# Kernel tuning notes

Hardware: AMD Instinct MI355X
Metric: run time of the kernel (lower is better)

The kernel has to match this reference:

```python
import jax, jax.numpy as jnp
import numpy as np

DIM = 512
EPS = 1e-08
LN_EPS = 1e-05  # torch LayerNorm default


def layer_norm(x, g, b):
    mu = jnp.mean(x, axis=-1, keepdims=True)
    var = jnp.mean(jnp.square(x - mu), axis=-1, keepdims=True)
    return (x - mu) * jax.lax.rsqrt(var + LN_EPS) * g + b


def setup_inputs() -> dict:
    key = jax.random.key(0)
    ks = jax.random.split(key, 10)
    B, NQ, NK, D = 8, 1024, 2048, DIM
    s = 1.0 / np.sqrt(D)
    return {
        "inputs": jax.random.normal(ks[0], (B, NQ, D), jnp.float32),
        "context": jax.random.normal(ks[1], (B, NK, D), jnp.float32),
        "ln_in_g": jnp.ones((D,), jnp.float32),
        "ln_in_b": jnp.zeros((D,), jnp.float32),
        "ln_ctx_g": jnp.ones((D,), jnp.float32),
        "ln_ctx_b": jnp.zeros((D,), jnp.float32),
        "Wq": jax.random.uniform(ks[2], (D, D), jnp.float32, -s, s),
        "bq": jax.random.uniform(ks[3], (D,), jnp.float32, -s, s),
        "Wk": jax.random.uniform(ks[4], (D, D), jnp.float32, -s, s),
        "bk": jax.random.uniform(ks[5], (D,), jnp.float32, -s, s),
        "Wv": jax.random.uniform(ks[6], (D, D), jnp.float32, -s, s),
        "bv": jax.random.uniform(ks[7], (D,), jnp.float32, -s, s),
    }


def reference(inputs, context, ln_in_g, ln_in_b, ln_ctx_g, ln_ctx_b, Wq, bq, Wk, bk, Wv, bv):
    x = layer_norm(inputs, ln_in_g, ln_in_b)
    c = layer_norm(context, ln_ctx_g, ln_ctx_b)
    q = x @ Wq.T + bq  # [B, Nq, D]
    k = c @ Wk.T + bk  # [B, Nk, D]
    v = c @ Wv.T + bv  # [B, Nk, D]
    scale = DIM ** (-0.5)
    dots = jnp.einsum('bid,bjd->bij', q, k) * scale  # [B, Nq, Nk]
    attn = jax.nn.softmax(dots, axis=1) + EPS  # softmax over query axis
    attn = attn / jnp.sum(attn, axis=2, keepdims=True)  # renorm over key axis
    updates = jnp.einsum('bjd,bij->bid', v, attn)
    return updates
```

## Files before the change

kernel.cpp:

```cpp
#include <hip/hip_runtime.h>

using u16 = unsigned short;
typedef __attribute__((ext_vector_type(8))) short short8;
typedef __attribute__((ext_vector_type(4))) float floatx4;

#define NQ 1024
#define NK 2048
#define DD 512

__device__ __forceinline__ u16 f2bf(float f) {
  union { float f; unsigned u; } x; x.f = f;
  unsigned r = (x.u + 0x7fffu + ((x.u >> 16) & 1u)) >> 16;
  return (u16)r;
}
__device__ __forceinline__ float bf2f(u16 u) {
  union { unsigned u; float f; } x; x.u = ((unsigned)u) << 16; return x.f;
}
__device__ __forceinline__ float wave_sum(float v) {
#pragma unroll
  for (int off = 32; off > 0; off >>= 1) v += __shfl_down(v, off, 64);
  return v;
}
__device__ __forceinline__ void gload16(const u16* g, const u16* l) {
  __builtin_amdgcn_global_load_lds(
      (const __attribute__((address_space(1))) void*)g,
      (__attribute__((address_space(3))) void*)l, 16, 0, 0);
}

__global__ __launch_bounds__(256) void ln_prep(
    const float* __restrict__ X1, const float* __restrict__ G1,
    const float* __restrict__ B1, u16* __restrict__ Y1,
    const float* __restrict__ X2, const float* __restrict__ G2,
    const float* __restrict__ B2, u16* __restrict__ Y2,
    const float* __restrict__ Wq, const float* __restrict__ Wk,
    const float* __restrict__ Wv, u16* __restrict__ wqb,
    u16* __restrict__ wkb, u16* __restrict__ wvb, float* __restrict__ Zero) {
  int row = blockIdx.x;
  const int t = threadIdx.x;
  if (row >= 24576) {
    int bx = row - 24576;
    if (bx < 768) {
      const float* src = bx < 256 ? Wq : (bx < 512 ? Wk : Wv);
      u16* dst = bx < 256 ? wqb : (bx < 512 ? wkb : wvb);
      int i = ((bx & 255) * 256 + t) * 4;
      float4 v = *(const float4*)(src + i);
      ushort4 o;
      o.x = f2bf(v.x); o.y = f2bf(v.y); o.z = f2bf(v.z); o.w = f2bf(v.w);
      *(ushort4*)(dst + i) = o;
    } else {
      int i = ((bx - 768) * 256 + t) * 4;
      float4 z = {0.f, 0.f, 0.f, 0.f};
      *(float4*)(Zero + i) = z;
    }
    return;
  }
  const float *X, *G, *Bv; u16* Y;
  if (row < 8192) { X = X1; G = G1; Bv = B1; Y = Y1; }
  else { row -= 8192; X = X2; G = G2; Bv = B2; Y = Y2; }
  const float2 v = ((const float2*)(X + (long)row * DD))[t];
  float s = v.x + v.y, ss = v.x * v.x + v.y * v.y;
  __shared__ float red[8];
  float a = wave_sum(s), b = wave_sum(ss);
  if ((t & 63) == 0) { red[t >> 6] = a; red[4 + (t >> 6)] = b; }
  __syncthreads();
  float tot = red[0] + red[1] + red[2] + red[3];
  float tss = red[4] + red[5] + red[6] + red[7];
  float mu = tot * (1.f / DD);
  float var = tss * (1.f / DD) - mu * mu;
  float rs = rsqrtf(var + 1e-5f);
  float2 g2 = ((const float2*)G)[t];
  float2 b2 = ((const float2*)Bv)[t];
  ushort2 o;
  o.x = f2bf((v.x - mu) * rs * g2.x + b2.x);
  o.y = f2bf((v.y - mu) * rs * g2.y + b2.y);
  ((ushort2*)(Y + (long)row * DD))[t] = o;
}

__global__ __launch_bounds__(256) void gemm_bt(
    const u16* A, const u16* B, const float* bias, void* Cout,
    const u16* A2, const u16* B2, const float* bias2, void* Cout2,
    int K, long sAb, long sBb, long sCb, int ldC,
    float scale, int epi, float* aux0, const float* aux1) {
  __shared__ u16 lA[128 * 64];
  __shared__ u16 lB[128 * 64];
  __shared__ float colred[128];

  int m0, n0, bz;
  if (epi == 3) {
    bz = blockIdx.x; m0 = blockIdx.z * 128; n0 = blockIdx.y * 128;
  } else {
    bz = blockIdx.z; m0 = blockIdx.x * 128; n0 = blockIdx.y * 128;
    if (A2 != nullptr && blockIdx.x >= 64) {
      A = A2; B = B2; bias = bias2; Cout = Cout2;
      m0 = (blockIdx.x - 64) * 128;
    }
  }
  A += (long)bz * sAb;
  B += (long)bz * sBb;
  const int t = threadIdx.x, wave = t >> 6, lane = t & 63;
  const int fm = lane & 15, fq = lane >> 4;
  const int wm = (wave >> 1) * 64, wn = (wave & 1) * 64;

  const int srow = t >> 3;
  const int swz = ((t & 7) ^ (srow & 7)) * 8;
  const u16* gA = A + (long)(m0 + srow) * K + swz;
  const u16* gB = B + (long)(n0 + srow) * K + swz;
  const long gk32 = 32L * K;
  u16* dA = lA + wave * 512;
  u16* dB = lB + wave * 512;

  floatx4 acc[4][4];
#pragma unroll
  for (int x = 0; x < 4; ++x)
#pragma unroll
    for (int y = 0; y < 4; ++y) { floatx4 z = {0.f, 0.f, 0.f, 0.f}; acc[x][y] = z; }

  const int nkt = K >> 6;
  for (int kt = 0; kt < nkt; ++kt) {
    gload16(gA, dA);
    gload16(gA + gk32, dA + 2048);
    gload16(gA + 2 * gk32, dA + 4096);
    gload16(gA + 3 * gk32, dA + 6144);
    gload16(gB, dB);
    gload16(gB + gk32, dB + 2048);
    gload16(gB + 2 * gk32, dB + 4096);
    gload16(gB + 3 * gk32, dB + 6144);
    gA += 64; gB += 64;
    __syncthreads();
#pragma unroll
    for (int ks = 0; ks < 2; ++ks) {
      short8 af[4], bfr[4];
      const int csl = ((ks * 4 + fq) ^ (fm & 7)) * 8;
#pragma unroll
      for (int x = 0; x < 4; ++x)
        af[x] = *(const short8*)&lA[(wm + x * 16 + fm) * 64 + csl];
#pragma unroll
      for (int y = 0; y < 4; ++y)
        bfr[y] = *(const short8*)&lB[(wn + y * 16 + fm) * 64 + csl];
#pragma unroll
      for (int x = 0; x < 4; ++x)
#pragma unroll
        for (int y = 0; y < 4; ++y)
          acc[x][y] = __builtin_amdgcn_mfma_f32_16x16x32_bf16(af[x], bfr[y], acc[x][y], 0, 0, 0);
    }
    __syncthreads();
  }

  if (epi == 0) {
    float bs[4];
#pragma unroll
    for (int y = 0; y < 4; ++y) bs[y] = bias[n0 + wn + y * 16 + fm];
#pragma unroll
    for (int x = 0; x < 4; ++x)
#pragma unroll
      for (int y = 0; y < 4; ++y)
#pragma unroll
        for (int r = 0; r < 4; ++r) {
          int row = m0 + wm + x * 16 + fq * 4 + r;
          int col = n0 + wn + y * 16 + fm;
          ((u16*)Cout)[(long)bz * sCb + (long)row * ldC + col] =
              f2bf(acc[x][y][r] + bs[y]);
        }
  } else if (epi == 3) {
    float s4[4] = {0.f, 0.f, 0.f, 0.f};
#pragma unroll
    for (int x = 0; x < 4; ++x)
#pragma unroll
      for (int y = 0; y < 4; ++y)
#pragma unroll
        for (int r = 0; r < 4; ++r) {
          int row = m0 + wm + x * 16 + fq * 4 + r;
          int col = n0 + wn + y * 16 + fm;
          float e = __expf(acc[x][y][r] * scale);
          s4[y] += e;
          ((u16*)Cout)[(long)bz * sCb + (long)row * ldC + col] = f2bf(e);
        }
#pragma unroll
    for (int y = 0; y < 4; ++y) {
      s4[y] += __shfl_xor(s4[y], 16, 64);
      s4[y] += __shfl_xor(s4[y], 32, 64);
    }
    if (t < 128) colred[t] = 0.f;
    __syncthreads();
    if (fq == 0) {
#pragma unroll
      for (int y = 0; y < 4; ++y) atomicAdd(&colred[wn + y * 16 + fm], s4[y]);
    }
    __syncthreads();
    if (t < 128) atomicAdd(&aux0[bz * 2048 + n0 + t], colred[t]);
  } else {
    const int bb = n0 >> 11;
    const int j0c = n0 & 2047;
    float bsr[4][4];
#pragma unroll
    for (int x = 0; x < 4; ++x)
#pragma unroll
      for (int r = 0; r < 4; ++r)
        bsr[x][r] = bias[m0 + wm + x * 16 + fq * 4 + r];
    float izv[4];
#pragma unroll
    for (int y = 0; y < 4; ++y)
      izv[y] = __builtin_amdgcn_rcpf(aux1[bb * 2048 + j0c + wn + y * 16 + fm]);
    u16* Cg = (u16*)Cout + (long)bb * (512L * 2048) + j0c;
    float rs[4][4];
#pragma unroll
    for (int x = 0; x < 4; ++x)
#pragma unroll
      for (int r = 0; r < 4; ++r) rs[x][r] = 0.f;
#pragma unroll
    for (int x = 0; x < 4; ++x)
#pragma unroll
      for (int y = 0; y < 4; ++y)
#pragma unroll
        for (int r = 0; r < 4; ++r) {
          int rowd = m0 + wm + x * 16 + fq * 4 + r;
          int col = wn + y * 16 + fm;
          float val = acc[x][y][r] + bsr[x][r];
          rs[x][r] += val;
          Cg[(long)rowd * 2048 + col] = f2bf(val * izv[y]);
        }
#pragma unroll
    for (int x = 0; x < 4; ++x)
#pragma unroll
      for (int r = 0; r < 4; ++r) {
        float s = rs[x][r];
        s += __shfl_xor(s, 1, 64);
        s += __shfl_xor(s, 2, 64);
        s += __shfl_xor(s, 4, 64);
        s += __shfl_xor(s, 8, 64);
        if (fm == 0)
          atomicAdd(&aux0[bb * 512 + m0 + wm + x * 16 + fq * 4 + r], s);
      }
  }
}

__global__ __launch_bounds__(256) void gemm_pv(const u16* __restrict__ E,
    const u16* __restrict__ V, const float* __restrict__ colV,
    const float* __restrict__ Z, float* __restrict__ out) {
  __shared__ u16 lA[64 * 64];
  __shared__ u16 lB[64 * 64];
  __shared__ u16 sZb[2048];
  const int b = blockIdx.z;
  const int m0 = blockIdx.x * 64, n0 = blockIdx.y * 64;
  const int t = threadIdx.x, wave = t >> 6, lane = t & 63;
  const int fm = lane & 15, fq = lane >> 4;
  const int wm = (wave >> 1) * 32, wn = (wave & 1) * 32;

  {
    int i = t * 8;
    float4 z0 = *(const float4*)(Z + b * 2048 + i);
    float4 z1 = *(const float4*)(Z + b * 2048 + i + 4);
    short8 o;
    o[0] = (short)f2bf(__builtin_amdgcn_rcpf(z0.x));
    o[1] = (short)f2bf(__builtin_amdgcn_rcpf(z0.y));
    o[2] = (short)f2bf(__builtin_amdgcn_rcpf(z0.z));
    o[3] = (short)f2bf(__builtin_amdgcn_rcpf(z0.w));
    o[4] = (short)f2bf(__builtin_amdgcn_rcpf(z1.x));
    o[5] = (short)f2bf(__builtin_amdgcn_rcpf(z1.y));
    o[6] = (short)f2bf(__builtin_amdgcn_rcpf(z1.z));
    o[7] = (short)f2bf(__builtin_amdgcn_rcpf(z1.w));
    *(short8*)&sZb[i] = o;
  }

  const int srow = t >> 3;
  const int swz = ((t & 7) ^ (srow & 7)) * 8;
  const u16* gA = E + (long)b * (1024L * 2048) + (long)(m0 + srow) * 2048 + swz;
  const u16* gB = V + (long)b * (512L * 2048) + (long)(n0 + srow) * 2048 + swz;
  u16* dA = lA + wave * 512;
  u16* dB = lB + wave * 512;

  floatx4 acc[2][2];
  floatx4 accR[2];
#pragma unroll
  for (int x = 0; x < 2; ++x) {
    floatx4 z = {0.f, 0.f, 0.f, 0.f};
    accR[x] = z;
#pragma unroll
    for (int y = 0; y < 2; ++y) acc[x][y] = z;
  }

  for (int kt = 0; kt < 32; ++kt) {
    gload16(gA, dA);
    gload16(gA + 32L * 2048, dA + 2048);
    gload16(gB, dB);
    gload16(gB + 32L * 2048, dB + 2048);
    gA += 64; gB += 64;
    __syncthreads();
#pragma unroll
    for (int ks = 0; ks < 2; ++ks) {
      short8 af[2], bfr[2];
      const int chunk = ks * 4 + fq;
      const int csl = (chunk ^ (fm & 7)) * 8;
#pragma unroll
      for (int x = 0; x < 2; ++x)
        af[x] = *(const short8*)&lA[(wm + x * 16 + fm) * 64 + csl];
#pragma unroll
      for (int y = 0; y < 2; ++y)
        bfr[y] = *(const short8*)&lB[(wn + y * 16 + fm) * 64 + csl];
      short8 zf = *(const short8*)&sZb[kt * 64 + chunk * 8];
#pragma unroll
      for (int x = 0; x < 2; ++x) {
#pragma unroll
        for (int y = 0; y < 2; ++y)
          acc[x][y] = __builtin_amdgcn_mfma_f32_16x16x32_bf16(af[x], bfr[y], acc[x][y], 0, 0, 0);
        accR[x] = __builtin_amdgcn_mfma_f32_16x16x32_bf16(af[x], zf, accR[x], 0, 0, 0);
      }
    }
    __syncthreads();
  }

  float cv[2];
#pragma unroll
  for (int y = 0; y < 2; ++y) cv[y] = colV[b * 512 + n0 + wn + y * 16 + fm];
  float* og = out + (long)b * (1024L * 512);
#pragma unroll
  for (int x = 0; x < 2; ++x)
#pragma unroll
    for (int r = 0; r < 4; ++r) {
      float invR = __builtin_amdgcn_rcpf(accR[x][r] + 2048.f * 1e-8f);
      int row = m0 + wm + x * 16 + fq * 4 + r;
#pragma unroll
      for (int y = 0; y < 2; ++y) {
        int col = n0 + wn + y * 16 + fm;
        og[(long)row * 512 + col] = (acc[x][y][r] + 1e-8f * cv[y]) * invR;
      }
    }
}

extern "C" void kernel_launch(void* const* d_in, const int* in_sizes, int n_in,
                              void* d_out, int out_size, void* d_ws, size_t ws_size,
                              hipStream_t stream) {
  const float* inputs  = (const float*)d_in[0];
  const float* context = (const float*)d_in[1];
  const float* ln_in_g = (const float*)d_in[2];
  const float* ln_in_b = (const float*)d_in[3];
  const float* ln_ctx_g = (const float*)d_in[4];
  const float* ln_ctx_b = (const float*)d_in[5];
  const float* Wq = (const float*)d_in[6];
  const float* bq = (const float*)d_in[7];
  const float* Wk = (const float*)d_in[8];
  const float* bk = (const float*)d_in[9];
  const float* Wv = (const float*)d_in[10];
  const float* bv = (const float*)d_in[11];
  float* out = (float*)d_out;

  u16* ws = (u16*)d_ws;
  u16* xb  = ws;
  u16* qb  = xb + 8192L * 512;
  u16* cb  = qb + 8192L * 512;
  u16* wqb = cb + 16384L * 512;
  u16* wkb = wqb + 512L * 512;
  u16* wvb = wkb + 512L * 512;
  u16* kb  = wvb + 512L * 512;
  u16* vTs = kb + 16384L * 512;
  u16* E   = vTs + 8L * 512 * 2048;
  float* Z    = (float*)(E + 8L * 1024 * 2048);
  float* colV = Z + 8L * 2048;

  const float scale = 0.04419417382415922f;

  ln_prep<<<25364, 256, 0, stream>>>(inputs, ln_in_g, ln_in_b, xb,
                                     context, ln_ctx_g, ln_ctx_b, cb,
                                     Wq, Wk, Wv, wqb, wkb, wvb, Z);
  gemm_bt<<<dim3(192, 4, 1), 256, 0, stream>>>(xb, wqb, bq, qb,
      cb, wkb, bk, kb, 512, 0L, 0L, 0L, 512, 1.0f, 0, nullptr, nullptr);
  gemm_bt<<<dim3(8, 16, 8), 256, 0, stream>>>(qb, kb, nullptr, E,
      nullptr, nullptr, nullptr, nullptr,
      512, 1024L * 512, 2048L * 512, 1024L * 2048, 2048, scale, 3, Z, nullptr);
  gemm_bt<<<dim3(4, 128, 1), 256, 0, stream>>>(wvb, cb, bv, vTs,
      nullptr, nullptr, nullptr, nullptr,
      512, 0L, 0L, 0L, 2048, 1.0f, 6, colV, Z);
  gemm_pv<<<dim3(16, 8, 8), 256, 0, stream>>>(E, vTs, colV, Z, out);
}
```

Baseline: 224.6 us.

## Merge QK-exp and V-projection into one launch, add separate V scaling pass

Splits the generic epilogue-switch GEMM into specialized kernels with hardcoded K=512. The QK^T+exp GEMM and the V projection GEMM now run in a single 1536-block launch, so the two independent workloads fill the GPU together. V's division by the column sums Z is moved into a separate elementwise scaleV pass, because Z is no longer complete when V is produced. Batch-fastest block indexing is also used in the QK and PV kernels. The cost is an extra read-modify-write pass over V plus one more launch.

```diff
diff --git a/kernel.cpp b/kernel.cpp
--- a/kernel.cpp
+++ b/kernel.cpp
@@ -76,36 +76,117 @@
   ((ushort2*)(Y + (long)row * DD))[t] = o;
 }
 
-__global__ __launch_bounds__(256) void gemm_bt(
-    const u16* A, const u16* B, const float* bias, void* Cout,
-    const u16* A2, const u16* B2, const float* bias2, void* Cout2,
-    int K, long sAb, long sBb, long sCb, int ldC,
-    float scale, int epi, float* aux0, const float* aux1) {
+__global__ __launch_bounds__(256) void gemm_proj(
+    const u16* __restrict__ A1, const u16* __restrict__ W1,
+    const float* __restrict__ b1, u16* __restrict__ C1,
+    const u16* __restrict__ A2, const u16* __restrict__ W2,
+    const float* __restrict__ b2, u16* __restrict__ C2) {
+  __shared__ u16 lA[128 * 64];
+  __shared__ u16 lB[128 * 64];
+  const u16 *A, *B; const float* bias; u16* Cout;
+  int m0 = blockIdx.x * 128;
+  if (blockIdx.x < 64) { A = A1; B = W1; bias = b1; Cout = C1; }
+  else { A = A2; B = W2; bias = b2; Cout = C2; m0 = (blockIdx.x - 64) * 128; }
+  const int n0 = blockIdx.y * 128;
+  const int t = threadIdx.x, wave = t >> 6, lane = t & 63;
+  const int fm = lane & 15, fq = lane >> 4;
+  const int wm = (wave >> 1) * 64, wn = (wave & 1) * 64;
+
+  const int srow = t >> 3;
+  const int swz = ((t & 7) ^ (srow & 7)) * 8;
+  const u16* gA = A + (long)(m0 + srow) * 512 + swz;
+  const u16* gB = B + (long)(n0 + srow) * 512 + swz;
+  u16* dA = lA + wave * 512;
+  u16* dB = lB + wave * 512;
+
+  floatx4 acc[4][4];
+#pragma unroll
+  for (int x = 0; x < 4; ++x)
+#pragma unroll
+    for (int y = 0; y < 4; ++y) { floatx4 z = {0.f, 0.f, 0.f, 0.f}; acc[x][y] = z; }
+
+#pragma unroll 1
+  for (int kt = 0; kt < 8; ++kt) {
+    gload16(gA, dA);
+    gload16(gA + 32L * 512, dA + 2048);
+    gload16(gA + 64L * 512, dA + 4096);
+    gload16(gA + 96L * 512, dA + 6144);
+    gload16(gB, dB);
+    gload16(gB + 32L * 512, dB + 2048);
+    gload16(gB + 64L * 512, dB + 4096);
+    gload16(gB + 96L * 512, dB + 6144);
+    gA += 64; gB += 64;
+    __syncthreads();
+#pragma unroll
+    for (int ks = 0; ks < 2; ++ks) {
+      short8 af[4], bfr[4];
+      const int csl = ((ks * 4 + fq) ^ (fm & 7)) * 8;
+#pragma unroll
+      for (int x = 0; x < 4; ++x)
+        af[x] = *(const short8*)&lA[(wm + x * 16 + fm) * 64 + csl];
+#pragma unroll
+      for (int y = 0; y < 4; ++y)
+        bfr[y] = *(const short8*)&lB[(wn + y * 16 + fm) * 64 + csl];
+#pragma unroll
+      for (int x = 0; x < 4; ++x)
+#pragma unroll
+        for (int y = 0; y < 4; ++y)
+          acc[x][y] = __builtin_amdgcn_mfma_f32_16x16x32_bf16(af[x], bfr[y], acc[x][y], 0, 0, 0);
+    }
+    __syncthreads();
+  }
+
+  float bs[4];
+#pragma unroll
+  for (int y = 0; y < 4; ++y) bs[y] = bias[n0 + wn + y * 16 + fm];
+#pragma unroll
+  for (int x = 0; x < 4; ++x)
+#pragma unroll
+    for (int y = 0; y < 4; ++y)
+#pragma unroll
+      for (int r = 0; r < 4; ++r) {
+        int row = m0 + wm + x * 16 + fq * 4 + r;
+        int col = n0 + wn + y * 16 + fm;
+        Cout[(long)row * 512 + col] = f2bf(acc[x][y][r] + bs[y]);
+      }
+}
+
+__global__ __launch_bounds__(256) void qk_vproj(
+    const u16* __restrict__ qb, const u16* __restrict__ kb,
+    u16* __restrict__ E, float* __restrict__ Z,
+    const u16* __restrict__ wvb, const u16* __restrict__ cb,
+    const float* __restrict__ bv, u16* __restrict__ vT,
+    float* __restrict__ colV, float scale) {
   __shared__ u16 lA[128 * 64];
   __shared__ u16 lB[128 * 64];
   __shared__ float colred[128];
 
-  int m0, n0, bz;
-  if (epi == 3) {
-    bz = blockIdx.x; m0 = blockIdx.z * 128; n0 = blockIdx.y * 128;
+  const int bx = blockIdx.x;
+  const bool is_qk = bx < 1024;
+  const u16 *A, *B;
+  int m0, n0, b;
+  if (is_qk) {
+    b = bx & 7;
+    n0 = ((bx >> 3) & 15) * 128;
+    m0 = (bx >> 7) * 128;
+    A = qb + (long)b * (1024L * 512);
+    B = kb + (long)b * (2048L * 512);
   } else {
-    bz = blockIdx.z; m0 = blockIdx.x * 128; n0 = blockIdx.y * 128;
-    if (A2 != nullptr && blockIdx.x >= 64) {
-      A = A2; B = B2; bias = bias2; Cout = Cout2;
-      m0 = (blockIdx.x - 64) * 128;
-    }
-  }
-  A += (long)bz * sAb;
-  B += (long)bz * sBb;
+    int e = bx - 1024;
+    m0 = (e & 3) * 128;
+    n0 = (e >> 2) * 128;
+    b = 0;
+    A = wvb;
+    B = cb;
+  }
   const int t = threadIdx.x, wave = t >> 6, lane = t & 63;
   const int fm = lane & 15, fq = lane >> 4;
   const int wm = (wave >> 1) * 64, wn = (wave & 1) * 64;
 
   const int srow = t >> 3;
   const int swz = ((t & 7) ^ (srow & 7)) * 8;
-  const u16* gA = A + (long)(m0 + srow) * K + swz;
-  const u16* gB = B + (long)(n0 + srow) * K + swz;
-  const long gk32 = 32L * K;
+  const u16* gA = A + (long)(m0 + srow) * 512 + swz;
+  const u16* gB = B + (long)(n0 + srow) * 512 + swz;
   u16* dA = lA + wave * 512;
   u16* dB = lB + wave * 512;
 
@@ -115,16 +196,16 @@
 #pragma unroll
     for (int y = 0; y < 4; ++y) { floatx4 z = {0.f, 0.f, 0.f, 0.f}; acc[x][y] = z; }
 
-  const int nkt = K >> 6;
-  for (int kt = 0; kt < nkt; ++kt) {
+#pragma unroll 1
+  for (int kt = 0; kt < 8; ++kt) {
     gload16(gA, dA);
-    gload16(gA + gk32, dA + 2048);
-    gload16(gA + 2 * gk32, dA + 4096);
-    gload16(gA + 3 * gk32, dA + 6144);
+    gload16(gA + 32L * 512, dA + 2048);
+    gload16(gA + 64L * 512, dA + 4096);
+    gload16(gA + 96L * 512, dA + 6144);
     gload16(gB, dB);
-    gload16(gB + gk32, dB + 2048);
-    gload16(gB + 2 * gk32, dB + 4096);
-    gload16(gB + 3 * gk32, dB + 6144);
+    gload16(gB + 32L * 512, dB + 2048);
+    gload16(gB + 64L * 512, dB + 4096);
+    gload16(gB + 96L * 512, dB + 6144);
     gA += 64; gB += 64;
     __syncthreads();
 #pragma unroll
@@ -146,23 +227,9 @@
     __syncthreads();
   }
 
-  if (epi == 0) {
-    float bs[4];
-#pragma unroll
-    for (int y = 0; y < 4; ++y) bs[y] = bias[n0 + wn + y * 16 + fm];
-#pragma unroll
-    for (int x = 0; x < 4; ++x)
-#pragma unroll
-      for (int y = 0; y < 4; ++y)
-#pragma unroll
-        for (int r = 0; r < 4; ++r) {
-          int row = m0 + wm + x * 16 + fq * 4 + r;
-          int col = n0 + wn + y * 16 + fm;
-          ((u16*)Cout)[(long)bz * sCb + (long)row * ldC + col] =
-              f2bf(acc[x][y][r] + bs[y]);
-        }
-  } else if (epi == 3) {
+  if (is_qk) {
     float s4[4] = {0.f, 0.f, 0.f, 0.f};
+    u16* Eg = E + (long)b * (1024L * 2048);
 #pragma unroll
     for (int x = 0; x < 4; ++x)
 #pragma unroll
@@ -173,7 +240,7 @@
           int col = n0 + wn + y * 16 + fm;
           float e = __expf(acc[x][y][r] * scale);
           s4[y] += e;
-          ((u16*)Cout)[(long)bz * sCb + (long)row * ldC + col] = f2bf(e);
+          Eg[(long)row * 2048 + col] = f2bf(e);
         }
 #pragma unroll
     for (int y = 0; y < 4; ++y) {
@@ -187,7 +254,7 @@
       for (int y = 0; y < 4; ++y) atomicAdd(&colred[wn + y * 16 + fm], s4[y]);
     }
     __syncthreads();
-    if (t < 128) atomicAdd(&aux0[bz * 2048 + n0 + t], colred[t]);
+    if (t < 128) atomicAdd(&Z[b * 2048 + n0 + t], colred[t]);
   } else {
     const int bb = n0 >> 11;
     const int j0c = n0 & 2047;
@@ -196,12 +263,8 @@
     for (int x = 0; x < 4; ++x)
 #pragma unroll
       for (int r = 0; r < 4; ++r)
-        bsr[x][r] = bias[m0 + wm + x * 16 + fq * 4 + r];
-    float izv[4];
-#pragma unroll
-    for (int y = 0; y < 4; ++y)
-      izv[y] = __builtin_amdgcn_rcpf(aux1[bb * 2048 + j0c + wn + y * 16 + fm]);
-    u16* Cg = (u16*)Cout + (long)bb * (512L * 2048) + j0c;
+        bsr[x][r] = bv[m0 + wm + x * 16 + fq * 4 + r];
+    u16* Cg = vT + (long)bb * (512L * 2048) + j0c;
     float rs[4][4];
 #pragma unroll
     for (int x = 0; x < 4; ++x)
@@ -217,7 +280,7 @@
           int col = wn + y * 16 + fm;
           float val = acc[x][y][r] + bsr[x][r];
           rs[x][r] += val;
-          Cg[(long)rowd * 2048 + col] = f2bf(val * izv[y]);
+          Cg[(long)rowd * 2048 + col] = f2bf(val);
         }
 #pragma unroll
     for (int x = 0; x < 4; ++x)
@@ -229,9 +292,23 @@
         s += __shfl_xor(s, 4, 64);
         s += __shfl_xor(s, 8, 64);
         if (fm == 0)
-          atomicAdd(&aux0[bb * 512 + m0 + wm + x * 16 + fq * 4 + r], s);
+          atomicAdd(&colV[bb * 512 + m0 + wm + x * 16 + fq * 4 + r], s);
       }
   }
+}
+
+__global__ __launch_bounds__(256) void scaleV(u16* __restrict__ vT,
+                                              const float* __restrict__ Z) {
+  const long f = ((long)blockIdx.x * 256 + threadIdx.x) * 8;
+  const int b = (int)(f >> 20);
+  const int j = (int)(f & 2047);
+  const float* zp = Z + b * 2048 + j;
+  short8 v = *(const short8*)(vT + f);
+  short8 o;
+#pragma unroll
+  for (int k = 0; k < 8; ++k)
+    o[k] = (short)f2bf(bf2f((u16)v[k]) * __builtin_amdgcn_rcpf(zp[k]));
+  *(short8*)(vT + f) = o;
 }
 
 __global__ __launch_bounds__(256) void gemm_pv(const u16* __restrict__ E,
@@ -240,8 +317,9 @@
   __shared__ u16 lA[64 * 64];
   __shared__ u16 lB[64 * 64];
   __shared__ u16 sZb[2048];
-  const int b = blockIdx.z;
-  const int m0 = blockIdx.x * 64, n0 = blockIdx.y * 64;
+  const int id = blockIdx.x;
+  const int b = id & 7;
+  const int m0 = ((id >> 3) & 15) * 64, n0 = (id >> 7) * 64;
   const int t = threadIdx.x, wave = t >> 6, lane = t & 63;
   const int fm = lane & 15, fq = lane >> 4;
   const int wm = (wave >> 1) * 32, wn = (wave & 1) * 32;
@@ -279,6 +357,7 @@
     for (int y = 0; y < 2; ++y) acc[x][y] = z;
   }
 
+#pragma unroll 1
   for (int kt = 0; kt < 32; ++kt) {
     gload16(gA, dA);
     gload16(gA + 32L * 2048, dA + 2048);
@@ -362,13 +441,10 @@
   ln_prep<<<25364, 256, 0, stream>>>(inputs, ln_in_g, ln_in_b, xb,
                                      context, ln_ctx_g, ln_ctx_b, cb,
                                      Wq, Wk, Wv, wqb, wkb, wvb, Z);
-  gemm_bt<<<dim3(192, 4, 1), 256, 0, stream>>>(xb, wqb, bq, qb,
-      cb, wkb, bk, kb, 512, 0L, 0L, 0L, 512, 1.0f, 0, nullptr, nullptr);
-  gemm_bt<<<dim3(8, 16, 8), 256, 0, stream>>>(qb, kb, nullptr, E,
-      nullptr, nullptr, nullptr, nullptr,
-      512, 1024L * 512, 2048L * 512, 1024L * 2048, 2048, scale, 3, Z, nullptr);
-  gemm_bt<<<dim3(4, 128, 1), 256, 0, stream>>>(wvb, cb, bv, vTs,
-      nullptr, nullptr, nullptr, nullptr,
-      512, 0L, 0L, 0L, 2048, 1.0f, 6, colV, Z);
-  gemm_pv<<<dim3(16, 8, 8), 256, 0, stream>>>(E, vTs, colV, Z, out);
-}
+  gemm_proj<<<dim3(192, 4, 1), 256, 0, stream>>>(xb, wqb, bq, qb,
+                                                 cb, wkb, bk, kb);
+  qk_vproj<<<1536, 256, 0, stream>>>(qb, kb, E, Z, wvb, cb, bv, vTs,
+                                     colV, scale);
+  scaleV<<<4096, 256, 0, stream>>>(vTs, Z);
+  gemm_pv<<<1024, 256, 0, stream>>>(E, vTs, colV, Z, out);
+}
```

Measured after the change: 226.4 us. About the same (+0.8%).
